# Kernel tuning notes

Measured on AMD Instinct MI355X. Metric: run time of the kernel, lower is better.

Reference implementation:

```python
import jax, jax.numpy as jnp
import numpy as np
from jax import lax

B, S, E, H = 4, 1024, 512, 8
D = E // H


def setup_inputs() -> dict:
    key = jax.random.key(0)
    k1, k2, k3 = jax.random.split(key, 3)
    source = jax.random.normal(k1, (B, S, E), dtype=jnp.float32)
    target = jax.random.normal(k2, (B, S, E), dtype=jnp.float32)
    # orthogonal-initialized positional encoder [1, H, 1, D]; random rows are a fine stand-in
    enc = jax.random.normal(k3, (1, H, 1, D), dtype=jnp.float32)
    enc = enc / jnp.linalg.norm(enc, axis=-1, keepdims=True)
    return {
        "source": source,
        "target": target,
        "encoder": enc,
        "alpha": jnp.float32(1.0),
        "beta": jnp.float32(1.0),
        "gamma": jnp.float32(2.0),
    }


def _split_heads(x):
    b, s, e = x.shape
    return x.reshape(b, s, H, e // H).transpose(0, 2, 1, 3)  # [B,H,S,D]


def reference(source, target, encoder, alpha, beta, gamma):
    q = _split_heads(source)  # [B,H,S,D]
    k = _split_heads(target)  # [B,H,S,D]
    pe = encoder[0, :, 0, :]  # [H,D]

    # --- grammar (time) attention: sequential tanh recurrence over t ---
    def step(cc, k_t):
        # cc, k_t: [B,H,D]
        cc = jnp.tanh(cc * pe)
        out = jnp.einsum('bhsd,bhd->bhs', q, cc)  # [B,H,S]
        return k_t * cc, out  # decay_rate = 0.0

    cc0 = k[:, :, 0, :]                      # initial cumulative context
    k_ts = jnp.moveaxis(k, 2, 0)             # [S,B,H,D]
    _, outs = lax.scan(step, cc0, k_ts)      # outs: [S,B,H,S]
    grammar = jnp.moveaxis(outs, 0, 3) / jnp.sqrt(jnp.float32(D))  # [B,H,S,S]
    grammar = jax.nn.softmax(grammar, axis=-1)

    # --- semantic attention ---
    semantic = jnp.einsum('bhsd,bhtd->bhst', q, k) / 100.0  # [B,H,S,S]

    w = jax.nn.softmax((alpha * semantic + beta * grammar) / gamma, axis=-1)

    # merge_heads: [B,H,S,S] -> [B,S,H*S]
    wm = w.transpose(0, 2, 1, 3).reshape(B, S, H * S)
    # output: wm^T @ target -> [B, H*S, E]
    return jnp.matmul(wm.transpose(0, 2, 1), target)
```

## Files before the change

kernel.cpp:

```cpp
#include <hip/hip_runtime.h>
#include <hip/hip_bf16.h>
#include <stdint.h>

#define S_LEN 1024
#define E_DIM 512
#define H_NUM 8
#define D_DIM 64
#define B_NUM 4
#define BH_NUM 32

using s16x8 = __attribute__((ext_vector_type(8))) short;
using f32x4 = __attribute__((ext_vector_type(4))) float;
using us4   = __attribute__((ext_vector_type(4))) unsigned short;

typedef const __attribute__((address_space(1))) uint32_t gas_uint;
typedef __attribute__((address_space(3))) uint32_t las_uint;

static __device__ __forceinline__ unsigned short f2bf(float f) {
  __hip_bfloat16 h = __float2bfloat16(f);
  return __builtin_bit_cast(unsigned short, h);
}
static __device__ __forceinline__ float bf2f(unsigned short u) {
  return __bfloat162float(__builtin_bit_cast(__hip_bfloat16, u));
}

#define NB_RECUR 8
#define NB_PACK  2048
#define NB_TR    512

__global__ __launch_bounds__(256) void k_prep(const float* __restrict__ src,
                                              const float* __restrict__ tgt,
                                              const float* __restrict__ enc,
                                              __hip_bfloat16* __restrict__ qb,
                                              __hip_bfloat16* __restrict__ kb,
                                              __hip_bfloat16* __restrict__ cb,
                                              __hip_bfloat16* __restrict__ tT) {
  __shared__ float tile[64][65];
  const int bid = blockIdx.x;
  const int tid = threadIdx.x;

  if (bid < NB_RECUR) {
    int g = bid * 256 + tid;
    int d = g & 63;
    int bh = g >> 6;
    int h = bh & 7;
    int b = bh >> 3;
    float pe = enc[h * D_DIM + d];
    float pe2 = 2.0f * pe;
    const float* tp = tgt + (size_t)b * S_LEN * E_DIM + h * D_DIM + d;
    __hip_bfloat16* cp = cb + (size_t)bh * S_LEN * D_DIM + d;

    constexpr int CH = 32;
    float bufA[CH], bufB[CH];
#pragma unroll
    for (int i = 0; i < CH; ++i) bufA[i] = tp[(size_t)i * E_DIM];
    float cc = bufA[0];

#pragma unroll 1
    for (int ch = 0; ch < S_LEN / CH; ch += 2) {
      if (ch + 1 < S_LEN / CH) {
#pragma unroll
        for (int i = 0; i < CH; ++i)
          bufB[i] = tp[(size_t)((ch + 1) * CH + i) * E_DIM];
      }
#pragma unroll
      for (int i = 0; i < CH; ++i) {
        float m = cc * pe2;
        float e = __expf(-fabsf(m));
        float th = __builtin_copysignf((1.0f - e) * __builtin_amdgcn_rcpf(1.0f + e), m);
        cp[(size_t)(ch * CH + i) * D_DIM] = __float2bfloat16(th);
        cc = bufA[i] * th;
      }
      if (ch + 2 < S_LEN / CH) {
#pragma unroll
        for (int i = 0; i < CH; ++i)
          bufA[i] = tp[(size_t)((ch + 2) * CH + i) * E_DIM];
      }
#pragma unroll
      for (int i = 0; i < CH; ++i) {
        float m = cc * pe2;
        float e = __expf(-fabsf(m));
        float th = __builtin_copysignf((1.0f - e) * __builtin_amdgcn_rcpf(1.0f + e), m);
        cp[(size_t)((ch + 1) * CH + i) * D_DIM] = __float2bfloat16(th);
        cc = bufB[i] * th;
      }
    }
  } else if (bid < NB_RECUR + NB_PACK) {
    size_t i4 = ((size_t)(bid - NB_RECUR) * 256 + tid) * 4;
    float4 s4 = *reinterpret_cast<const float4*>(src + i4);
    float4 t4 = *reinterpret_cast<const float4*>(tgt + i4);
    int e = (int)(i4 & 511);
    size_t bs = i4 >> 9;
    int s = (int)(bs & 1023);
    int b = (int)(bs >> 10);
    int h = e >> 6, d = e & 63;
    size_t o = (((size_t)(b * H_NUM + h) * S_LEN) + s) * D_DIM + d;
    us4 qv = {f2bf(s4.x), f2bf(s4.y), f2bf(s4.z), f2bf(s4.w)};
    us4 kv = {f2bf(t4.x), f2bf(t4.y), f2bf(t4.z), f2bf(t4.w)};
    *reinterpret_cast<us4*>(qb + o) = qv;
    *reinterpret_cast<us4*>(kb + o) = kv;
  } else {
    int lb = bid - (NB_RECUR + NB_PACK);
    int sx = lb & 15, ey = (lb >> 4) & 7, b = lb >> 7;
    int e0 = ey * 64, s0 = sx * 64;
    int tx = tid & 63, ty = tid >> 6;
    const float* p = tgt + ((size_t)b * S_LEN + s0) * E_DIM + e0;
#pragma unroll
    for (int r = ty; r < 64; r += 4) tile[r][tx] = p[(size_t)r * E_DIM + tx];
    __syncthreads();
    __hip_bfloat16* q = tT + ((size_t)b * E_DIM + e0) * S_LEN + s0;
#pragma unroll
    for (int r = ty; r < 64; r += 4) q[(size_t)r * S_LEN + tx] = __float2bfloat16(tile[tx][r]);
  }
}

__global__ __launch_bounds__(512) void k_weights(const __hip_bfloat16* __restrict__ qb,
                                                 const __hip_bfloat16* __restrict__ kb,
                                                 const __hip_bfloat16* __restrict__ cb,
                                                 __hip_bfloat16* __restrict__ wt,
                                                 const float* __restrict__ pal,
                                                 const float* __restrict__ pbe,
                                                 const float* __restrict__ pga) {
  __shared__ unsigned short stage[8][3][2048];
  __shared__ float red0[8][32];
  __shared__ float red1[8][32];

  const int tid = threadIdx.x;
  const int wave = tid >> 6, lane = tid & 63;
  const int quad = lane >> 4, col = lane & 15;

  const int g = blockIdx.x;
  const int xcd = g & 7;
  const int r = g >> 3;
  const int bh = xcd * 4 + (r >> 5);
  const int s0 = (r & 31) * 32;

  const float alpha = pal[0], beta = pbe[0];
  const float inv_gamma = 1.0f / pga[0];
  const float sa = alpha * 0.01f * inv_gamma;
  const float sb = beta * inv_gamma;

  const __hip_bfloat16* qrow = qb + ((size_t)bh * S_LEN + s0 + col) * D_DIM;
  s16x8 a0 = *reinterpret_cast<const s16x8*>(qrow + quad * 8);
  s16x8 a1 = *reinterpret_cast<const s16x8*>(qrow + 32 + quad * 8);
  s16x8 a2 = *reinterpret_cast<const s16x8*>(qrow + 16 * D_DIM + quad * 8);
  s16x8 a3 = *reinterpret_cast<const s16x8*>(qrow + 16 * D_DIM + 32 + quad * 8);

  const int t_base = wave * 128;
  uint32_t stg0[8][2], stg1[8][2];
  float    stk0[8][4], stk1[8][4];

  const char* cbase = (const char*)(cb + ((size_t)bh * S_LEN + t_base) * D_DIM);
  const char* kbase = (const char*)(kb + ((size_t)bh * S_LEN + t_base) * D_DIM);
  const int so0 = ((lane >> 3) << 7) | (((lane & 7) ^ ((lane >> 3) & 7)) << 4);

  auto stage_it = [&](int it) {
    unsigned short* db = &stage[wave][it % 3][0];
    const char* cs = cbase + it * 2048;
    const char* ks = kbase + it * 2048;
    __builtin_amdgcn_global_load_lds((gas_uint*)(cs + so0),        (las_uint*)(db),        16, 0, 0);
    __builtin_amdgcn_global_load_lds((gas_uint*)(cs + so0 + 1024), (las_uint*)(db + 512),  16, 0, 0);
    __builtin_amdgcn_global_load_lds((gas_uint*)(ks + so0),        (las_uint*)(db + 1024), 16, 0, 0);
    __builtin_amdgcn_global_load_lds((gas_uint*)(ks + so0 + 1024), (las_uint*)(db + 1536), 16, 0, 0);
  };

  stage_it(0);
  stage_it(1);

  const int xswz = (col & 7) << 4;
  float lg0[4] = {0.f, 0.f, 0.f, 0.f};
  float lg1[4] = {0.f, 0.f, 0.f, 0.f};
#pragma unroll
  for (int it = 0; it < 8; ++it) {
    if (it < 7) asm volatile("s_waitcnt vmcnt(4)" ::: "memory");
    else        asm volatile("s_waitcnt vmcnt(0)" ::: "memory");
    const char* cw = (const char*)&stage[wave][it % 3][0];
    const char* kw = cw + 2048;
    const int rb = col * 128;
    s16x8 cf0 = *reinterpret_cast<const s16x8*>(cw + rb + ((quad * 16) ^ xswz));
    s16x8 cf1 = *reinterpret_cast<const s16x8*>(cw + rb + ((64 + quad * 16) ^ xswz));
    s16x8 kf0 = *reinterpret_cast<const s16x8*>(kw + rb + ((quad * 16) ^ xswz));
    s16x8 kf1 = *reinterpret_cast<const s16x8*>(kw + rb + ((64 + quad * 16) ^ xswz));
    f32x4 dg0 = {0.f, 0.f, 0.f, 0.f};
    f32x4 dg1 = {0.f, 0.f, 0.f, 0.f};
    f32x4 dk0 = {0.f, 0.f, 0.f, 0.f};
    f32x4 dk1 = {0.f, 0.f, 0.f, 0.f};
    __builtin_amdgcn_s_setprio(1);
    dg0 = __builtin_amdgcn_mfma_f32_16x16x32_bf16(a0, cf0, dg0, 0, 0, 0);
    dg0 = __builtin_amdgcn_mfma_f32_16x16x32_bf16(a1, cf1, dg0, 0, 0, 0);
    dg1 = __builtin_amdgcn_mfma_f32_16x16x32_bf16(a2, cf0, dg1, 0, 0, 0);
    dg1 = __builtin_amdgcn_mfma_f32_16x16x32_bf16(a3, cf1, dg1, 0, 0, 0);
    dk0 = __builtin_amdgcn_mfma_f32_16x16x32_bf16(a0, kf0, dk0, 0, 0, 0);
    dk0 = __builtin_amdgcn_mfma_f32_16x16x32_bf16(a1, kf1, dk0, 0, 0, 0);
    dk1 = __builtin_amdgcn_mfma_f32_16x16x32_bf16(a2, kf0, dk1, 0, 0, 0);
    dk1 = __builtin_amdgcn_mfma_f32_16x16x32_bf16(a3, kf1, dk1, 0, 0, 0);
    __builtin_amdgcn_s_setprio(0);
    if (it + 2 < 8) stage_it(it + 2);
    uint32_t p0 = 0, p1 = 0, q0 = 0, q1 = 0;
#pragma unroll
    for (int i = 0; i < 4; ++i) {
      float gv0 = __expf(dg0[i] * 0.125f);
      float gv1 = __expf(dg1[i] * 0.125f);
      unsigned short u0 = f2bf(gv0);
      unsigned short u1 = f2bf(gv1);
      lg0[i] += bf2f(u0);
      lg1[i] += bf2f(u1);
      if (i < 2) { p0 |= (uint32_t)u0 << (16 * i);       q0 |= (uint32_t)u1 << (16 * i); }
      else       { p1 |= (uint32_t)u0 << (16 * (i - 2)); q1 |= (uint32_t)u1 << (16 * (i - 2)); }
      stk0[it][i] = dk0[i];
      stk1[it][i] = dk1[i];
    }
    stg0[it][0] = p0; stg0[it][1] = p1;
    stg1[it][0] = q0; stg1[it][1] = q1;
  }
#pragma unroll
  for (int m = 1; m < 16; m <<= 1) {
#pragma unroll
    for (int i = 0; i < 4; ++i) {
      lg0[i] += __shfl_xor(lg0[i], m);
      lg1[i] += __shfl_xor(lg1[i], m);
    }
  }
  if (col == 0) {
#pragma unroll
    for (int i = 0; i < 4; ++i) {
      red0[wave][quad * 4 + i]      = lg0[i];
      red0[wave][16 + quad * 4 + i] = lg1[i];
    }
  }
  __syncthreads();
  float ilg0[4], ilg1[4];
#pragma unroll
  for (int i = 0; i < 4; ++i) {
    int r0 = quad * 4 + i, r1 = 16 + quad * 4 + i;
    float s0a = 0.f, s1a = 0.f;
#pragma unroll
    for (int w = 0; w < 8; ++w) { s0a += red0[w][r0]; s1a += red0[w][r1]; }
    ilg0[i] = 1.0f / s0a;
    ilg1[i] = 1.0f / s1a;
  }

  float lw0[4] = {0.f, 0.f, 0.f, 0.f};
  float lw1[4] = {0.f, 0.f, 0.f, 0.f};
#pragma unroll
  for (int it = 0; it < 8; ++it) {
#pragma unroll
    for (int i = 0; i < 4; ++i) {
      unsigned short u0 = (unsigned short)((i < 2 ? stg0[it][0] >> (16 * i)
                                                  : stg0[it][1] >> (16 * (i - 2))) & 0xffffu);
      unsigned short u1 = (unsigned short)((i < 2 ? stg1[it][0] >> (16 * i)
                                                  : stg1[it][1] >> (16 * (i - 2))) & 0xffffu);
      float gv0 = bf2f(u0) * ilg0[i];
      float gv1 = bf2f(u1) * ilg1[i];
      float z0 = sa * stk0[it][i] + sb * gv0;
      float z1 = sa * stk1[it][i] + sb * gv1;
      float wv0 = __expf(z0);
      float wv1 = __expf(z1);
      stk0[it][i] = wv0;
      stk1[it][i] = wv1;
      lw0[i] += wv0;
      lw1[i] += wv1;
    }
  }
#pragma unroll
  for (int m = 1; m < 16; m <<= 1) {
#pragma unroll
    for (int i = 0; i < 4; ++i) {
      lw0[i] += __shfl_xor(lw0[i], m);
      lw1[i] += __shfl_xor(lw1[i], m);
    }
  }
  if (col == 0) {
#pragma unroll
    for (int i = 0; i < 4; ++i) {
      red1[wave][quad * 4 + i]      = lw0[i];
      red1[wave][16 + quad * 4 + i] = lw1[i];
    }
  }
  __syncthreads();
  float ilw0[4], ilw1[4];
#pragma unroll
  for (int i = 0; i < 4; ++i) {
    int r0 = quad * 4 + i, r1 = 16 + quad * 4 + i;
    float s0a = 0.f, s1a = 0.f;
#pragma unroll
    for (int w = 0; w < 8; ++w) { s0a += red1[w][r0]; s1a += red1[w][r1]; }
    ilw0[i] = 1.0f / s0a;
    ilw1[i] = 1.0f / s1a;
  }

  __hip_bfloat16* wrow = wt + ((size_t)bh * S_LEN + t_base + col) * S_LEN + s0 + quad * 4;
#pragma unroll
  for (int it = 0; it < 8; ++it) {
    us4 o0, o1;
#pragma unroll
    for (int i = 0; i < 4; ++i) {
      o0[i] = f2bf(stk0[it][i] * ilw0[i]);
      o1[i] = f2bf(stk1[it][i] * ilw1[i]);
    }
    *reinterpret_cast<us4*>(wrow + (size_t)it * 16 * S_LEN)      = o0;
    *reinterpret_cast<us4*>(wrow + (size_t)it * 16 * S_LEN + 16) = o1;
  }
}

__global__ __launch_bounds__(256) void k_outgemm(const __hip_bfloat16* __restrict__ wt,
                                                 const __hip_bfloat16* __restrict__ tT,
                                                 float* __restrict__ out) {
  __shared__ __hip_bfloat16 As[2][128 * 64];
  __shared__ __hip_bfloat16 Bs[2][128 * 64];
  const int tid = threadIdx.x;
  const int wave = tid >> 6, lane = tid & 63;
  const int quad = lane >> 4, col = lane & 15;

  const int g = blockIdx.x;
  const int xcd = g & 7;
  const int local = g >> 3;
  const int strip = xcd * 32 + (local >> 2);
  const int ntile = local & 3;
  const int bh = strip >> 3;
  const int mt = strip & 7;
  const int b = bh >> 3;
  const int m0 = mt * 128;
  const int n0 = ntile * 128;

  const __hip_bfloat16* Ag = wt + (size_t)bh * S_LEN * S_LEN;
  const __hip_bfloat16* Bg = tT + (size_t)b * E_DIM * S_LEN;
  const int mw = (wave >> 1) * 64, nw = (wave & 1) * 64;
  const int lrow = lane >> 3;
  const int lcolswz = ((lane & 7) ^ lrow) * 8;

  f32x4 acc[4][4];
#pragma unroll
  for (int i = 0; i < 4; ++i)
#pragma unroll
    for (int j = 0; j < 4; ++j) acc[i][j] = (f32x4){0.f, 0.f, 0.f, 0.f};

  auto stage = [&](int kt, int buf) {
    const int k0 = kt * 64;
#pragma unroll
    for (int j = 0; j < 4; ++j) {
      const int rbase = j * 32 + wave * 8;
      const __hip_bfloat16* gpA = Ag + (size_t)(m0 + rbase + lrow) * S_LEN + k0 + lcolswz;
      __builtin_amdgcn_global_load_lds((gas_uint*)gpA,
                                       (las_uint*)(&As[buf][rbase * 64]), 16, 0, 0);
      const __hip_bfloat16* gpB = Bg + (size_t)(n0 + rbase + lrow) * S_LEN + k0 + lcolswz;
      __builtin_amdgcn_global_load_lds((gas_uint*)gpB,
                                       (las_uint*)(&Bs[buf][rbase * 64]), 16, 0, 0);
    }
  };

  const int swz = (col & 7) << 4;
  auto compute = [&](int buf) {
    const char* Ab = (const char*)&As[buf][0];
    const char* Bb = (const char*)&Bs[buf][0];
    __builtin_amdgcn_s_setprio(1);
#pragma unroll
    for (int ks = 0; ks < 2; ++ks) {
      s16x8 af[4], bfr[4];
#pragma unroll
      for (int i = 0; i < 4; ++i)
        af[i] = *reinterpret_cast<const s16x8*>(
            Ab + (size_t)(mw + i * 16 + col) * 128 + ((ks * 64 + quad * 16) ^ swz));
#pragma unroll
      for (int i = 0; i < 4; ++i)
        bfr[i] = *reinterpret_cast<const s16x8*>(
            Bb + (size_t)(nw + i * 16 + col) * 128 + ((ks * 64 + quad * 16) ^ swz));
#pragma unroll
      for (int mi = 0; mi < 4; ++mi)
#pragma unroll
        for (int ni = 0; ni < 4; ++ni)
          acc[mi][ni] = __builtin_amdgcn_mfma_f32_16x16x32_bf16(af[mi], bfr[ni], acc[mi][ni], 0, 0, 0);
    }
    __builtin_amdgcn_s_setprio(0);
  };

  stage(0, 0);
#pragma unroll 1
  for (int kt = 0; kt < 15; ++kt) {
    stage(kt + 1, (kt + 1) & 1);
    asm volatile("s_waitcnt vmcnt(8)" ::: "memory");
    __builtin_amdgcn_s_barrier();
    compute(kt & 1);
    asm volatile("" ::: "memory");
    __builtin_amdgcn_s_barrier();
  }
  asm volatile("s_waitcnt vmcnt(0)" ::: "memory");
  __builtin_amdgcn_s_barrier();
  compute(1);

#pragma unroll
  for (int mi = 0; mi < 4; ++mi)
#pragma unroll
    for (int ni = 0; ni < 4; ++ni)
#pragma unroll
      for (int i = 0; i < 4; ++i) {
        int m = m0 + mw + mi * 16 + quad * 4 + i;
        int n = n0 + nw + ni * 16 + col;
        out[((size_t)bh * S_LEN + m) * E_DIM + n] = acc[mi][ni][i];
      }
}

extern "C" void kernel_launch(void* const* d_in, const int* in_sizes, int n_in,
                              void* d_out, int out_size, void* d_ws, size_t ws_size,
                              hipStream_t stream) {
  (void)in_sizes; (void)n_in; (void)out_size; (void)ws_size;
  const float* src = (const float*)d_in[0];
  const float* tgt = (const float*)d_in[1];
  const float* enc = (const float*)d_in[2];
  const float* pal = (const float*)d_in[3];
  const float* pbe = (const float*)d_in[4];
  const float* pga = (const float*)d_in[5];
  float* out = (float*)d_out;

  char* ws = (char*)d_ws;
  __hip_bfloat16* qb = (__hip_bfloat16*)(ws);
  __hip_bfloat16* kb = (__hip_bfloat16*)(ws + ((size_t)4 << 20));
  __hip_bfloat16* cb = (__hip_bfloat16*)(ws + ((size_t)8 << 20));
  __hip_bfloat16* tT = (__hip_bfloat16*)(ws + ((size_t)12 << 20));
  __hip_bfloat16* wt = (__hip_bfloat16*)(ws + ((size_t)16 << 20));

  k_prep<<<NB_RECUR + NB_PACK + NB_TR, 256, 0, stream>>>(src, tgt, enc, qb, kb, cb, tT);
  k_weights<<<dim3((S_LEN / 32) * BH_NUM), 512, 0, stream>>>(qb, kb, cb, wt, pal, pbe, pga);
  k_outgemm<<<dim3((E_DIM / 128) * (S_LEN / 128) * BH_NUM), 256, 0, stream>>>(wt, tT, out);
}
```

Before: 207.4 us.

## Split staging into half-tiles to halve LDS buffer and deepen pipeline

The per-wave LDS staging ring now holds a single 2 KB half-tile (either the C tile or the K tile) instead of both together, which halves the shared memory footprint of the weights kernel. Loads are issued per half-tile with three in flight, and the C and K MFMA groups each get their own wait and prefetch point, with sched barriers to keep the order fixed. The aim is finer-grained overlap of global-to-LDS loads with MFMA work and possibly higher occupancy, at the cost of more waitcnt points and a more fragile vmcnt accounting.

```diff
diff --git a/kernel.cpp b/kernel.cpp
--- a/kernel.cpp
+++ b/kernel.cpp
@@ -121,7 +121,7 @@
                                                  const float* __restrict__ pal,
                                                  const float* __restrict__ pbe,
                                                  const float* __restrict__ pga) {
-  __shared__ unsigned short stage[8][3][2048];
+  __shared__ unsigned short stage[8][3][1024];
   __shared__ float red0[8][32];
   __shared__ float red1[8][32];
 
@@ -154,48 +154,55 @@
   const char* kbase = (const char*)(kb + ((size_t)bh * S_LEN + t_base) * D_DIM);
   const int so0 = ((lane >> 3) << 7) | (((lane & 7) ^ ((lane >> 3) & 7)) << 4);
 
-  auto stage_it = [&](int it) {
-    unsigned short* db = &stage[wave][it % 3][0];
-    const char* cs = cbase + it * 2048;
-    const char* ks = kbase + it * 2048;
-    __builtin_amdgcn_global_load_lds((gas_uint*)(cs + so0),        (las_uint*)(db),        16, 0, 0);
-    __builtin_amdgcn_global_load_lds((gas_uint*)(cs + so0 + 1024), (las_uint*)(db + 512),  16, 0, 0);
-    __builtin_amdgcn_global_load_lds((gas_uint*)(ks + so0),        (las_uint*)(db + 1024), 16, 0, 0);
-    __builtin_amdgcn_global_load_lds((gas_uint*)(ks + so0 + 1024), (las_uint*)(db + 1536), 16, 0, 0);
+  auto stage_h = [&](int h) {
+    unsigned short* db = &stage[wave][h % 3][0];
+    const char* src = ((h & 1) ? kbase : cbase) + (h >> 1) * 2048;
+    __builtin_amdgcn_global_load_lds((gas_uint*)(src + so0),        (las_uint*)(db),       16, 0, 0);
+    __builtin_amdgcn_global_load_lds((gas_uint*)(src + so0 + 1024), (las_uint*)(db + 512), 16, 0, 0);
   };
 
-  stage_it(0);
-  stage_it(1);
+  stage_h(0);
+  stage_h(1);
+  stage_h(2);
 
   const int xswz = (col & 7) << 4;
+  const int rb = col * 128;
   float lg0[4] = {0.f, 0.f, 0.f, 0.f};
   float lg1[4] = {0.f, 0.f, 0.f, 0.f};
 #pragma unroll
   for (int it = 0; it < 8; ++it) {
     if (it < 7) asm volatile("s_waitcnt vmcnt(4)" ::: "memory");
-    else        asm volatile("s_waitcnt vmcnt(0)" ::: "memory");
-    const char* cw = (const char*)&stage[wave][it % 3][0];
-    const char* kw = cw + 2048;
-    const int rb = col * 128;
-    s16x8 cf0 = *reinterpret_cast<const s16x8*>(cw + rb + ((quad * 16) ^ xswz));
-    s16x8 cf1 = *reinterpret_cast<const s16x8*>(cw + rb + ((64 + quad * 16) ^ xswz));
-    s16x8 kf0 = *reinterpret_cast<const s16x8*>(kw + rb + ((quad * 16) ^ xswz));
-    s16x8 kf1 = *reinterpret_cast<const s16x8*>(kw + rb + ((64 + quad * 16) ^ xswz));
+    else        asm volatile("s_waitcnt vmcnt(2)" ::: "memory");
+    const char* cw = (const char*)&stage[wave][(2 * it) % 3][0];
+    s16x8 cf0 = *reinterpret_cast<const s16x8*>(cw + ((quad * 16) ^ xswz) + rb);
+    s16x8 cf1 = *reinterpret_cast<const s16x8*>(cw + ((64 + quad * 16) ^ xswz) + rb);
     f32x4 dg0 = {0.f, 0.f, 0.f, 0.f};
     f32x4 dg1 = {0.f, 0.f, 0.f, 0.f};
-    f32x4 dk0 = {0.f, 0.f, 0.f, 0.f};
-    f32x4 dk1 = {0.f, 0.f, 0.f, 0.f};
     __builtin_amdgcn_s_setprio(1);
     dg0 = __builtin_amdgcn_mfma_f32_16x16x32_bf16(a0, cf0, dg0, 0, 0, 0);
     dg0 = __builtin_amdgcn_mfma_f32_16x16x32_bf16(a1, cf1, dg0, 0, 0, 0);
     dg1 = __builtin_amdgcn_mfma_f32_16x16x32_bf16(a2, cf0, dg1, 0, 0, 0);
     dg1 = __builtin_amdgcn_mfma_f32_16x16x32_bf16(a3, cf1, dg1, 0, 0, 0);
+    __builtin_amdgcn_s_setprio(0);
+    __builtin_amdgcn_sched_barrier(0);
+    if (2 * it + 3 < 16) stage_h(2 * it + 3);
+
+    if (it < 7) asm volatile("s_waitcnt vmcnt(4)" ::: "memory");
+    else        asm volatile("s_waitcnt vmcnt(0)" ::: "memory");
+    const char* kw = (const char*)&stage[wave][(2 * it + 1) % 3][0];
+    s16x8 kf0 = *reinterpret_cast<const s16x8*>(kw + ((quad * 16) ^ xswz) + rb);
+    s16x8 kf1 = *reinterpret_cast<const s16x8*>(kw + ((64 + quad * 16) ^ xswz) + rb);
+    f32x4 dk0 = {0.f, 0.f, 0.f, 0.f};
+    f32x4 dk1 = {0.f, 0.f, 0.f, 0.f};
+    __builtin_amdgcn_s_setprio(1);
     dk0 = __builtin_amdgcn_mfma_f32_16x16x32_bf16(a0, kf0, dk0, 0, 0, 0);
     dk0 = __builtin_amdgcn_mfma_f32_16x16x32_bf16(a1, kf1, dk0, 0, 0, 0);
     dk1 = __builtin_amdgcn_mfma_f32_16x16x32_bf16(a2, kf0, dk1, 0, 0, 0);
     dk1 = __builtin_amdgcn_mfma_f32_16x16x32_bf16(a3, kf1, dk1, 0, 0, 0);
     __builtin_amdgcn_s_setprio(0);
-    if (it + 2 < 8) stage_it(it + 2);
+    __builtin_amdgcn_sched_barrier(0);
+    if (2 * it + 4 < 16) stage_h(2 * it + 4);
+
     uint32_t p0 = 0, p1 = 0, q0 = 0, q1 = 0;
 #pragma unroll
     for (int i = 0; i < 4; ++i) {
```

Result: no change. 208.4 us (+0.5%).
